# Kernel tuning notes

Hardware: AMD Instinct MI355X
Metric: run time of the kernel (lower is better)

## Reference

```python
import jax, jax.numpy as jnp
import numpy as np

B, L, HID, H, D = 16, 512, 768, 12, 64
NUM_STRUCT = 5


def setup_inputs() -> dict:
    key = jax.random.key(0)
    ks = jax.random.split(key, 8)
    hidden_states = jax.random.normal(ks[0], (B, L, HID), jnp.float32)
    attention_mask = jnp.zeros((B, 1, 1, L), jnp.float32)  # additive mask (0 = keep)
    structure_mask = (jax.random.uniform(ks[1], (NUM_STRUCT, B, 1, L, L)) < 0.15).astype(jnp.float32)
    s = 1.0 / np.sqrt(HID).astype(np.float32)
    Wq = jax.random.normal(ks[2], (HID, HID), jnp.float32) * s
    Wk = jax.random.normal(ks[3], (HID, HID), jnp.float32) * s
    Wv = jax.random.normal(ks[4], (HID, HID), jnp.float32) * s
    bq = jnp.zeros((HID,), jnp.float32)
    bk = jnp.zeros((HID,), jnp.float32)
    bv = jnp.zeros((HID,), jnp.float32)
    # xavier-uniform-ish scale for [D,D] biaffine mats
    xav = np.sqrt(6.0 / (D + D)).astype(np.float32)
    bili = jax.random.uniform(ks[5], (NUM_STRUCT, H, D, D), jnp.float32, -xav, xav)
    abs_bias = jnp.zeros((NUM_STRUCT, H), jnp.float32)
    return {"hidden_states": hidden_states, "attention_mask": attention_mask,
            "structure_mask": structure_mask, "Wq": Wq, "bq": bq, "Wk": Wk,
            "bk": bk, "Wv": Wv, "bv": bv, "bili": bili, "abs_bias": abs_bias}


def _heads(x, b, l):
    # [B,L,HID] -> [B,H,L,D]
    return x.reshape(b, l, H, D).transpose(0, 2, 1, 3)


def reference(hidden_states, attention_mask, structure_mask, Wq, bq, Wk, bk, Wv, bv, bili, abs_bias):
    b, l, _ = hidden_states.shape
    q = _heads(hidden_states @ Wq.T + bq, b, l)  # [B,H,L,D]
    k = _heads(hidden_states @ Wk.T + bk, b, l)
    v = _heads(hidden_states @ Wv.T + bv, b, l)

    scores = jnp.einsum('bhid,bhjd->bhij', q, k)  # [B,H,L,L]
    for i in range(NUM_STRUCT):
        bias = jnp.einsum('bhip,hpq,bhjq->bhij', q, bili[i], k)
        scores = scores + (bias + abs_bias[i][None, :, None, None]) * structure_mask[i]

    scores = scores / np.sqrt(D).astype(np.float32) + attention_mask
    probs = jax.nn.softmax(scores, axis=-1)
    ctx = jnp.einsum('bhij,bhjd->bhid', probs, v)  # [B,H,L,D]
    return ctx.transpose(0, 2, 1, 3).reshape(b, l, H * D)
```

## Files before the change

kernel.cpp:

```cpp
#include <hip/hip_runtime.h>
#include <hip/hip_bf16.h>

#define BATCH 16
#define SEQ   512
#define HID   768
#define NH    12
#define HD    64
#define NS    5

typedef __attribute__((ext_vector_type(8))) short short8;
typedef __attribute__((ext_vector_type(4))) float floatx4;

#define MFMA16(a, b, c) __builtin_amdgcn_mfma_f32_16x16x32_bf16((a), (b), (c), 0, 0, 0)

static __device__ __forceinline__ short f2bs(float f) {
    unsigned x = __builtin_bit_cast(unsigned, f);
    unsigned r = (x + 0x7fffu + ((x >> 16) & 1u)) >> 16;
    return (short)r;
}

__global__ void cvt_kernel(const float* __restrict__ src, short* __restrict__ dst, int n8) {
    int i = blockIdx.x * 256 + threadIdx.x;
    if (i >= n8) return;
    float4 a = ((const float4*)src)[2 * i];
    float4 b = ((const float4*)src)[2 * i + 1];
    short8 o;
    o[0] = f2bs(a.x); o[1] = f2bs(a.y); o[2] = f2bs(a.z); o[3] = f2bs(a.w);
    o[4] = f2bs(b.x); o[5] = f2bs(b.y); o[6] = f2bs(b.z); o[7] = f2bs(b.w);
    ((short8*)dst)[i] = o;
}

__global__ void bilit_kernel(const float* __restrict__ bili, short* __restrict__ bt) {
    int sh = blockIdx.x;
    const float* src = bili + (size_t)sh * 4096;
    short* dst = bt + (size_t)sh * 4096;
    for (int t = threadIdx.x; t < 4096; t += 256) {
        int p = t >> 6, qq = t & 63;
        dst[qq * 64 + p] = f2bs(src[p * 64 + qq]);
    }
}

__global__ void pack_mask_kernel(const float* __restrict__ smask, unsigned char* __restrict__ mp) {
    int idx = blockIdx.x * 256 + threadIdx.x;
    const size_t BLL = (size_t)BATCH * SEQ * SEQ;
    unsigned m = 0;
#pragma unroll
    for (int s = 0; s < NS; ++s)
        m |= (smask[(size_t)s * BLL + idx] != 0.f) ? (1u << s) : 0u;
    mp[idx] = (unsigned char)m;
}

__global__ __launch_bounds__(256) void proj_mfma(
    const short* __restrict__ xb, const short* __restrict__ Wb,
    const float* __restrict__ bq, const float* __restrict__ bk, const float* __restrict__ bv,
    short* __restrict__ qo, short* __restrict__ ko, short* __restrict__ vto)
{
    __shared__ short As[64 * 40];
    __shared__ short Bs[64 * 40];

    const int tid = threadIdx.x;
    const int m0 = blockIdx.x * 64;
    const int mh = blockIdx.y;
    const int mat = mh / NH, h = mh % NH;
    const short* Wm = Wb + (size_t)mat * HID * HID + (size_t)h * 64 * HID;
    const float* bias = (mat == 0) ? bq : (mat == 1) ? bk : bv;

    const int lane = tid & 63, w = tid >> 6;
    const int q4 = lane >> 4, c15 = lane & 15;
    const int srow = tid >> 2, skq = (tid & 3) * 8;

    floatx4 acc[4] = {{0.f,0.f,0.f,0.f},{0.f,0.f,0.f,0.f},{0.f,0.f,0.f,0.f},{0.f,0.f,0.f,0.f}};

    for (int k0 = 0; k0 < HID; k0 += 32) {
        *(short8*)&As[srow * 40 + skq] = *(const short8*)&xb[(size_t)(m0 + srow) * HID + k0 + skq];
        *(short8*)&Bs[srow * 40 + skq] = *(const short8*)&Wm[(size_t)srow * HID + k0 + skq];
        __syncthreads();
        short8 a = *(const short8*)&As[(w * 16 + c15) * 40 + q4 * 8];
#pragma unroll
        for (int c = 0; c < 4; ++c) {
            short8 bfr = *(const short8*)&Bs[(c * 16 + c15) * 40 + q4 * 8];
            acc[c] = MFMA16(a, bfr, acc[c]);
        }
        __syncthreads();
    }

    const int mg0 = m0 + w * 16 + q4 * 4;
    const int bb = mg0 >> 9, l0 = mg0 & 511;
#pragma unroll
    for (int c = 0; c < 4; ++c) {
        float bvv = bias[h * 64 + c * 16 + c15];
        if (mat < 2) {
            short* dst = (mat == 0) ? qo : ko;
#pragma unroll
            for (int r = 0; r < 4; ++r)
                dst[(((size_t)bb * NH + h) * SEQ + (l0 + r)) * HD + c * 16 + c15] = f2bs(acc[c][r] + bvv);
        } else {
            unsigned u0 = (unsigned short)f2bs(acc[c][0] + bvv) | ((unsigned)(unsigned short)f2bs(acc[c][1] + bvv) << 16);
            unsigned u1 = (unsigned short)f2bs(acc[c][2] + bvv) | ((unsigned)(unsigned short)f2bs(acc[c][3] + bvv) << 16);
            uint2 pk; pk.x = u0; pk.y = u1;
            *(uint2*)&vto[(((size_t)bb * NH + h) * HD + c * 16 + c15) * SEQ + l0] = pk;
        }
    }
}

__global__ __launch_bounds__(256, 3) void attn_mfma(
    const short* __restrict__ q, const short* __restrict__ k, const short* __restrict__ vt,
    const unsigned char* __restrict__ mp, const float* __restrict__ amask,
    const short* __restrict__ bilit, const float* __restrict__ abs_bias,
    float* __restrict__ out)
{
    __shared__ short Qs[64 * 72];
    __shared__ short Ks[64 * 72];
    __shared__ short Vs[64 * 72];
    __shared__ short Ps[64 * 72];

    const int it = blockIdx.x, h = blockIdx.y, b = blockIdx.z;
    const int i0 = it * 64;
    const int tid = threadIdx.x, lane = tid & 63, w = tid >> 6;
    const int q4 = lane >> 4, c15 = lane & 15;

    const size_t bh = (size_t)b * NH + h;
    const short* qg = q + bh * SEQ * HD;
    const short* kg = k + bh * SEQ * HD;
    const short* vg = vt + bh * HD * SEQ;

    for (int c = tid; c < 512; c += 256) {
        int r = c >> 3, o = (c & 7) * 8;
        *(short8*)&Qs[r * 72 + o] = *(const short8*)&qg[(size_t)(i0 + r) * HD + o];
    }
    float ab[NS];
#pragma unroll
    for (int s = 0; s < NS; ++s) ab[s] = abs_bias[s * NH + h];
    __syncthreads();

    short8 aQ0 = *(const short8*)&Qs[(w * 16 + c15) * 72 + q4 * 8];
    short8 aQ1 = *(const short8*)&Qs[(w * 16 + c15) * 72 + 32 + q4 * 8];

    short8 aP[NS][2];
    for (int s = 0; s < NS; ++s) {
        __syncthreads();
        const short* bt = bilit + ((size_t)s * NH + h) * 4096;
        for (int c = tid; c < 512; c += 256) {
            int r = c >> 3, o = (c & 7) * 8;
            *(short8*)&Ks[r * 72 + o] = *(const short8*)&bt[r * 64 + o];
        }
        __syncthreads();
#pragma unroll
        for (int ns = 0; ns < 4; ++ns) {
            short8 bf0 = *(const short8*)&Ks[(ns * 16 + c15) * 72 + q4 * 8];
            short8 bf1 = *(const short8*)&Ks[(ns * 16 + c15) * 72 + 32 + q4 * 8];
            floatx4 acc = {0.f, 0.f, 0.f, 0.f};
            acc = MFMA16(aQ0, bf0, acc);
            acc = MFMA16(aQ1, bf1, acc);
#pragma unroll
            for (int r = 0; r < 4; ++r)
                Ps[(w * 16 + q4 * 4 + r) * 72 + ns * 16 + c15] = f2bs(acc[r]);
        }
        aP[s][0] = *(const short8*)&Ps[(w * 16 + c15) * 72 + q4 * 8];
        aP[s][1] = *(const short8*)&Ps[(w * 16 + c15) * 72 + 32 + q4 * 8];
    }

    float m_r[4], l_r[4];
    floatx4 O[4];
#pragma unroll
    for (int r = 0; r < 4; ++r) { m_r[r] = -1e30f; l_r[r] = 0.f; }
#pragma unroll
    for (int d = 0; d < 4; ++d) O[d] = (floatx4){0.f, 0.f, 0.f, 0.f};

    const size_t mbase = (size_t)b * SEQ * SEQ;
    const int ibase = i0 + w * 16 + q4 * 4;

    for (int jt = 0; jt < 8; ++jt) {
        const int j0 = jt * 64;
        __syncthreads();
        for (int c = tid; c < 512; c += 256) {
            int r = c >> 3, o = (c & 7) * 8;
            *(short8*)&Ks[r * 72 + o] = *(const short8*)&kg[(size_t)(j0 + r) * HD + o];
            *(short8*)&Vs[r * 72 + o] = *(const short8*)&vg[(size_t)r * SEQ + j0 + o];
        }
        __syncthreads();

        float sv[4][4];
#pragma unroll
        for (int js = 0; js < 4; ++js) {
            const int jg = j0 + js * 16 + c15;
            unsigned mb[4];
#pragma unroll
            for (int r = 0; r < 4; ++r)
                mb[r] = mp[mbase + (size_t)(ibase + r) * SEQ + jg];
            float am = amask[b * SEQ + jg];

            short8 bf0 = *(const short8*)&Ks[(js * 16 + c15) * 72 + q4 * 8];
            short8 bf1 = *(const short8*)&Ks[(js * 16 + c15) * 72 + 32 + q4 * 8];
            floatx4 a0 = {0.f, 0.f, 0.f, 0.f};
            a0 = MFMA16(aQ0, bf0, a0);
            a0 = MFMA16(aQ1, bf1, a0);
            floatx4 as_[NS];
#pragma unroll
            for (int s = 0; s < NS; ++s) {
                floatx4 t = {0.f, 0.f, 0.f, 0.f};
                t = MFMA16(aP[s][0], bf0, t);
                t = MFMA16(aP[s][1], bf1, t);
                as_[s] = t;
            }
#pragma unroll
            for (int r = 0; r < 4; ++r) {
                float sc = a0[r];
#pragma unroll
                for (int s = 0; s < NS; ++s) {
                    float bit = (float)((mb[r] >> s) & 1u);
                    sc += bit * (as_[s][r] + ab[s]);
                }
                sv[js][r] = sc * 0.125f + am;
            }
        }

#pragma unroll
        for (int r = 0; r < 4; ++r) {
            float mx = fmaxf(fmaxf(sv[0][r], sv[1][r]), fmaxf(sv[2][r], sv[3][r]));
            mx = fmaxf(mx, __shfl_xor(mx, 1));
            mx = fmaxf(mx, __shfl_xor(mx, 2));
            mx = fmaxf(mx, __shfl_xor(mx, 4));
            mx = fmaxf(mx, __shfl_xor(mx, 8));
            float mn = fmaxf(m_r[r], mx);
            float alpha = __expf(m_r[r] - mn);
            m_r[r] = mn;
            float rs = 0.f;
#pragma unroll
            for (int js = 0; js < 4; ++js) {
                float p = __expf(sv[js][r] - mn);
                sv[js][r] = p;
                rs += p;
            }
            rs += __shfl_xor(rs, 1);
            rs += __shfl_xor(rs, 2);
            rs += __shfl_xor(rs, 4);
            rs += __shfl_xor(rs, 8);
            l_r[r] = l_r[r] * alpha + rs;
#pragma unroll
            for (int d = 0; d < 4; ++d) O[d][r] *= alpha;
        }

#pragma unroll
        for (int js = 0; js < 4; ++js)
#pragma unroll
            for (int r = 0; r < 4; ++r)
                Ps[(w * 16 + q4 * 4 + r) * 72 + js * 16 + c15] = f2bs(sv[js][r]);

        short8 pA0 = *(const short8*)&Ps[(w * 16 + c15) * 72 + q4 * 8];
        short8 pA1 = *(const short8*)&Ps[(w * 16 + c15) * 72 + 32 + q4 * 8];
#pragma unroll
        for (int d = 0; d < 4; ++d) {
            short8 vb0 = *(const short8*)&Vs[(d * 16 + c15) * 72 + q4 * 8];
            short8 vb1 = *(const short8*)&Vs[(d * 16 + c15) * 72 + 32 + q4 * 8];
            O[d] = MFMA16(pA0, vb0, O[d]);
            O[d] = MFMA16(pA1, vb1, O[d]);
        }
    }

#pragma unroll
    for (int r = 0; r < 4; ++r) {
        float inv = 1.f / l_r[r];
        int i = ibase + r;
        float* orow = out + ((size_t)b * SEQ + i) * HID + h * HD;
#pragma unroll
        for (int d = 0; d < 4; ++d)
            orow[d * 16 + c15] = O[d][r] * inv;
    }
}

extern "C" void kernel_launch(void* const* d_in, const int* in_sizes, int n_in,
                              void* d_out, int out_size, void* d_ws, size_t ws_size,
                              hipStream_t stream) {
    const float* hidden   = (const float*)d_in[0];
    const float* amask    = (const float*)d_in[1];
    const float* smask    = (const float*)d_in[2];
    const float* Wq       = (const float*)d_in[3];
    const float* bq       = (const float*)d_in[4];
    const float* Wk       = (const float*)d_in[5];
    const float* bk       = (const float*)d_in[6];
    const float* Wv       = (const float*)d_in[7];
    const float* bv       = (const float*)d_in[8];
    const float* bili     = (const float*)d_in[9];
    const float* abs_bias = (const float*)d_in[10];
    float* out = (float*)d_out;

    char* ws = (char*)d_ws;
    const size_t QKV = (size_t)BATCH * NH * SEQ * HD * 2;
    short* qb   = (short*)(ws);
    short* kb   = (short*)(ws + QKV);
    short* vtb  = (short*)(ws + 2 * QKV);
    short* xb   = (short*)(ws + 3 * QKV);
    short* Wb   = (short*)(ws + 4 * QKV);
    short* bltb = (short*)(ws + 4 * QKV + (size_t)3 * HID * HID * 2);
    unsigned char* mpk = (unsigned char*)(ws + 4 * QKV + (size_t)3 * HID * HID * 2
                                          + (size_t)NS * NH * HD * HD * 2);

    cvt_kernel<<<(BATCH * SEQ * HID / 8 + 255) / 256, 256, 0, stream>>>(hidden, xb, BATCH * SEQ * HID / 8);
    cvt_kernel<<<(HID * HID / 8 + 255) / 256, 256, 0, stream>>>(Wq, Wb, HID * HID / 8);
    cvt_kernel<<<(HID * HID / 8 + 255) / 256, 256, 0, stream>>>(Wk, Wb + (size_t)HID * HID, HID * HID / 8);
    cvt_kernel<<<(HID * HID / 8 + 255) / 256, 256, 0, stream>>>(Wv, Wb + (size_t)2 * HID * HID, HID * HID / 8);
    bilit_kernel<<<NS * NH, 256, 0, stream>>>(bili, bltb);
    pack_mask_kernel<<<BATCH * SEQ * SEQ / 256, 256, 0, stream>>>(smask, mpk);

    proj_mfma<<<dim3(BATCH * SEQ / 64, 3 * NH), 256, 0, stream>>>(xb, Wb, bq, bk, bv, qb, kb, vtb);

    attn_mfma<<<dim3(SEQ / 64, NH, BATCH), 256, 0, stream>>>(qb, kb, vtb, mpk, amask, bltb, abs_bias, out);
}
```

Baseline: 355.4 us.

## Retile projection GEMM, widen attention key tiles, vectorize mask packing, fold scales

The QKV projection moves from 64x64 tiles to 128x128 tiles per block, with a 4x4 MFMA grid per wave and direct global-to-LDS loads. The attention kernel now processes 128-key tiles, reuses one LDS buffer for Q, P and probabilities, and folds the 1/sqrt(D) scale into Q. The absolute biases are precomputed into a 32-entry lookup table indexed by the mask bits. Mask packing reads float4 and writes uchar4, and the three weight conversions are merged into one launch. Together these aim to cut global traffic, launch count and ALU work in the score loop, at the cost of more registers and LDS per block and possible occupancy loss.

```diff
diff --git a/kernel.cpp b/kernel.cpp
--- a/kernel.cpp
+++ b/kernel.cpp
@@ -13,10 +13,13 @@
 
 #define MFMA16(a, b, c) __builtin_amdgcn_mfma_f32_16x16x32_bf16((a), (b), (c), 0, 0, 0)
 
+#define GLOAD16(gp, lp) __builtin_amdgcn_global_load_lds( \
+    (const __attribute__((address_space(1))) unsigned*)(gp), \
+    (__attribute__((address_space(3))) unsigned*)(lp), 16, 0, 0)
+
 static __device__ __forceinline__ short f2bs(float f) {
     unsigned x = __builtin_bit_cast(unsigned, f);
-    unsigned r = (x + 0x7fffu + ((x >> 16) & 1u)) >> 16;
-    return (short)r;
+    return (short)((x + 0x7fffu + ((x >> 16) & 1u)) >> 16);
 }
 
 __global__ void cvt_kernel(const float* __restrict__ src, short* __restrict__ dst, int n8) {
@@ -30,6 +33,19 @@
     ((short8*)dst)[i] = o;
 }
 
+__global__ void cvtW_kernel(const float* __restrict__ wq, const float* __restrict__ wk,
+                            const float* __restrict__ wv, short* __restrict__ dst) {
+    const float* src = (blockIdx.y == 0) ? wq : (blockIdx.y == 1) ? wk : wv;
+    int i = blockIdx.x * 256 + threadIdx.x;
+    if (i >= HID * HID / 8) return;
+    float4 a = ((const float4*)src)[2 * i];
+    float4 b = ((const float4*)src)[2 * i + 1];
+    short8 o;
+    o[0] = f2bs(a.x); o[1] = f2bs(a.y); o[2] = f2bs(a.z); o[3] = f2bs(a.w);
+    o[4] = f2bs(b.x); o[5] = f2bs(b.y); o[6] = f2bs(b.z); o[7] = f2bs(b.w);
+    ((short8*)(dst + (size_t)blockIdx.y * HID * HID))[i] = o;
+}
+
 __global__ void bilit_kernel(const float* __restrict__ bili, short* __restrict__ bt) {
     int sh = blockIdx.x;
     const float* src = bili + (size_t)sh * 4096;
@@ -40,14 +56,20 @@
     }
 }
 
-__global__ void pack_mask_kernel(const float* __restrict__ smask, unsigned char* __restrict__ mp) {
-    int idx = blockIdx.x * 256 + threadIdx.x;
-    const size_t BLL = (size_t)BATCH * SEQ * SEQ;
-    unsigned m = 0;
-#pragma unroll
-    for (int s = 0; s < NS; ++s)
-        m |= (smask[(size_t)s * BLL + idx] != 0.f) ? (1u << s) : 0u;
-    mp[idx] = (unsigned char)m;
+__global__ void pack_mask_kernel(const float* __restrict__ smask, uchar4* __restrict__ mp) {
+    int i = blockIdx.x * 256 + threadIdx.x;
+    const size_t BLL4 = (size_t)BATCH * SEQ * SEQ / 4;
+    const float4* f = (const float4*)smask;
+    unsigned b0 = 0, b1 = 0, b2 = 0, b3 = 0;
+#pragma unroll
+    for (int s = 0; s < NS; ++s) {
+        float4 v = f[(size_t)s * BLL4 + i];
+        b0 |= (v.x != 0.f) ? (1u << s) : 0u;
+        b1 |= (v.y != 0.f) ? (1u << s) : 0u;
+        b2 |= (v.z != 0.f) ? (1u << s) : 0u;
+        b3 |= (v.w != 0.f) ? (1u << s) : 0u;
+    }
+    mp[i] = make_uchar4((unsigned char)b0, (unsigned char)b1, (unsigned char)b2, (unsigned char)b3);
 }
 
 __global__ __launch_bounds__(256) void proj_mfma(
@@ -55,64 +77,93 @@
     const float* __restrict__ bq, const float* __restrict__ bk, const float* __restrict__ bv,
     short* __restrict__ qo, short* __restrict__ ko, short* __restrict__ vto)
 {
-    __shared__ short As[64 * 40];
-    __shared__ short Bs[64 * 40];
-
-    const int tid = threadIdx.x;
-    const int m0 = blockIdx.x * 64;
-    const int mh = blockIdx.y;
-    const int mat = mh / NH, h = mh % NH;
-    const short* Wm = Wb + (size_t)mat * HID * HID + (size_t)h * 64 * HID;
-    const float* bias = (mat == 0) ? bq : (mat == 1) ? bk : bv;
-
-    const int lane = tid & 63, w = tid >> 6;
+    __shared__ short As[128 * 32];
+    __shared__ short Bs[128 * 32];
+
+    const int tid = threadIdx.x, lane = tid & 63, w = tid >> 6;
     const int q4 = lane >> 4, c15 = lane & 15;
-    const int srow = tid >> 2, skq = (tid & 3) * 8;
-
-    floatx4 acc[4] = {{0.f,0.f,0.f,0.f},{0.f,0.f,0.f,0.f},{0.f,0.f,0.f,0.f},{0.f,0.f,0.f,0.f}};
+    const int m0 = blockIdx.x * 128, n0 = blockIdx.y * 128;
+    const int wrow = (w & 1) * 64, wcol = (w >> 1) * 64;
+
+    const int srow = lane >> 2;
+    const int scol = (lane & 3) * 8;
+    const short* gA = xb + (size_t)(m0 + w * 32 + srow) * HID + scol;
+    const short* gB = Wb + (size_t)(n0 + w * 32 + srow) * HID + scol;
+    short* lA = As + w * 1024;
+    short* lB = Bs + w * 1024;
+
+    floatx4 acc[4][4];
+#pragma unroll
+    for (int i = 0; i < 4; ++i)
+#pragma unroll
+        for (int j = 0; j < 4; ++j) acc[i][j] = (floatx4){0.f, 0.f, 0.f, 0.f};
 
     for (int k0 = 0; k0 < HID; k0 += 32) {
-        *(short8*)&As[srow * 40 + skq] = *(const short8*)&xb[(size_t)(m0 + srow) * HID + k0 + skq];
-        *(short8*)&Bs[srow * 40 + skq] = *(const short8*)&Wm[(size_t)srow * HID + k0 + skq];
-        __syncthreads();
-        short8 a = *(const short8*)&As[(w * 16 + c15) * 40 + q4 * 8];
-#pragma unroll
-        for (int c = 0; c < 4; ++c) {
-            short8 bfr = *(const short8*)&Bs[(c * 16 + c15) * 40 + q4 * 8];
-            acc[c] = MFMA16(a, bfr, acc[c]);
-        }
-        __syncthreads();
-    }
-
-    const int mg0 = m0 + w * 16 + q4 * 4;
-    const int bb = mg0 >> 9, l0 = mg0 & 511;
-#pragma unroll
-    for (int c = 0; c < 4; ++c) {
-        float bvv = bias[h * 64 + c * 16 + c15];
-        if (mat < 2) {
-            short* dst = (mat == 0) ? qo : ko;
-#pragma unroll
-            for (int r = 0; r < 4; ++r)
-                dst[(((size_t)bb * NH + h) * SEQ + (l0 + r)) * HD + c * 16 + c15] = f2bs(acc[c][r] + bvv);
-        } else {
-            unsigned u0 = (unsigned short)f2bs(acc[c][0] + bvv) | ((unsigned)(unsigned short)f2bs(acc[c][1] + bvv) << 16);
-            unsigned u1 = (unsigned short)f2bs(acc[c][2] + bvv) | ((unsigned)(unsigned short)f2bs(acc[c][3] + bvv) << 16);
-            uint2 pk; pk.x = u0; pk.y = u1;
-            *(uint2*)&vto[(((size_t)bb * NH + h) * HD + c * 16 + c15) * SEQ + l0] = pk;
-        }
-    }
-}
-
-__global__ __launch_bounds__(256, 3) void attn_mfma(
+        __syncthreads();
+        GLOAD16(gA + k0,             lA);
+        GLOAD16(gA + k0 + 16 * HID,  lA + 512);
+        GLOAD16(gB + k0,             lB);
+        GLOAD16(gB + k0 + 16 * HID,  lB + 512);
+        __syncthreads();
+
+        short8 af[4], bf[4];
+#pragma unroll
+        for (int ri = 0; ri < 4; ++ri)
+            af[ri] = *(const short8*)&As[(wrow + ri * 16 + c15) * 32 + q4 * 8];
+#pragma unroll
+        for (int ci = 0; ci < 4; ++ci)
+            bf[ci] = *(const short8*)&Bs[(wcol + ci * 16 + c15) * 32 + q4 * 8];
+#pragma unroll
+        for (int ri = 0; ri < 4; ++ri)
+#pragma unroll
+            for (int ci = 0; ci < 4; ++ci)
+                acc[ri][ci] = MFMA16(af[ri], bf[ci], acc[ri][ci]);
+    }
+
+    const int matq = n0 / HID;
+    const float* bias = (matq == 0) ? bq : (matq == 1) ? bk : bv;
+
+#pragma unroll
+    for (int ci = 0; ci < 4; ++ci) {
+        const int nm = (n0 - matq * HID) + wcol + ci * 16 + c15;
+        const int h = nm >> 6, d = nm & 63;
+        const float bvv = bias[nm];
+#pragma unroll
+        for (int ri = 0; ri < 4; ++ri) {
+            const int mg0 = m0 + wrow + ri * 16 + q4 * 4;
+            const int bb = mg0 >> 9, l0 = mg0 & 511;
+            if (matq == 0) {
+#pragma unroll
+                for (int r = 0; r < 4; ++r)
+                    qo[(((size_t)bb * NH + h) * SEQ + (l0 + r)) * HD + d] =
+                        f2bs((acc[ri][ci][r] + bvv) * 0.125f);
+            } else if (matq == 1) {
+#pragma unroll
+                for (int r = 0; r < 4; ++r)
+                    ko[(((size_t)bb * NH + h) * SEQ + (l0 + r)) * HD + d] =
+                        f2bs(acc[ri][ci][r] + bvv);
+            } else {
+                unsigned u0 = (unsigned short)f2bs(acc[ri][ci][0] + bvv) |
+                              ((unsigned)(unsigned short)f2bs(acc[ri][ci][1] + bvv) << 16);
+                unsigned u1 = (unsigned short)f2bs(acc[ri][ci][2] + bvv) |
+                              ((unsigned)(unsigned short)f2bs(acc[ri][ci][3] + bvv) << 16);
+                uint2 pk; pk.x = u0; pk.y = u1;
+                *(uint2*)&vto[(((size_t)bb * NH + h) * HD + d) * SEQ + l0] = pk;
+            }
+        }
+    }
+}
+
+__global__ __launch_bounds__(256) void attn_mfma(
     const short* __restrict__ q, const short* __restrict__ k, const short* __restrict__ vt,
     const unsigned char* __restrict__ mp, const float* __restrict__ amask,
     const short* __restrict__ bilit, const float* __restrict__ abs_bias,
     float* __restrict__ out)
 {
-    __shared__ short Qs[64 * 72];
-    __shared__ short Ks[64 * 72];
-    __shared__ short Vs[64 * 72];
-    __shared__ short Ps[64 * 72];
+    __shared__ short U0[64 * 136];
+    __shared__ short Ks[128 * 72];
+    __shared__ short Vs[64 * 136];
+    __shared__ float abt[32];
 
     const int it = blockIdx.x, h = blockIdx.y, b = blockIdx.z;
     const int i0 = it * 64;
@@ -124,17 +175,21 @@
     const short* kg = k + bh * SEQ * HD;
     const short* vg = vt + bh * HD * SEQ;
 
+    if (tid < 32) {
+        float a = 0.f;
+#pragma unroll
+        for (int s = 0; s < NS; ++s)
+            if (tid & (1u << s)) a += abs_bias[s * NH + h];
+        abt[tid] = a * 0.125f;
+    }
+
     for (int c = tid; c < 512; c += 256) {
         int r = c >> 3, o = (c & 7) * 8;
-        *(short8*)&Qs[r * 72 + o] = *(const short8*)&qg[(size_t)(i0 + r) * HD + o];
-    }
-    float ab[NS];
-#pragma unroll
-    for (int s = 0; s < NS; ++s) ab[s] = abs_bias[s * NH + h];
+        *(short8*)&U0[r * 72 + o] = *(const short8*)&qg[(size_t)(i0 + r) * HD + o];
+    }
     __syncthreads();
-
-    short8 aQ0 = *(const short8*)&Qs[(w * 16 + c15) * 72 + q4 * 8];
-    short8 aQ1 = *(const short8*)&Qs[(w * 16 + c15) * 72 + 32 + q4 * 8];
+    short8 aQ0 = *(const short8*)&U0[(w * 16 + c15) * 72 + q4 * 8];
+    short8 aQ1 = *(const short8*)&U0[(w * 16 + c15) * 72 + 32 + q4 * 8];
 
     short8 aP[NS][2];
     for (int s = 0; s < NS; ++s) {
@@ -154,10 +209,10 @@
             acc = MFMA16(aQ1, bf1, acc);
 #pragma unroll
             for (int r = 0; r < 4; ++r)
-                Ps[(w * 16 + q4 * 4 + r) * 72 + ns * 16 + c15] = f2bs(acc[r]);
-        }
-        aP[s][0] = *(const short8*)&Ps[(w * 16 + c15) * 72 + q4 * 8];
-        aP[s][1] = *(const short8*)&Ps[(w * 16 + c15) * 72 + 32 + q4 * 8];
+                U0[(w * 16 + q4 * 4 + r) * 136 + ns * 16 + c15] = f2bs(acc[r]);
+        }
+        aP[s][0] = *(const short8*)&U0[(w * 16 + c15) * 136 + q4 * 8];
+        aP[s][1] = *(const short8*)&U0[(w * 16 + c15) * 136 + 32 + q4 * 8];
     }
 
     float m_r[4], l_r[4];
@@ -167,31 +222,31 @@
 #pragma unroll
     for (int d = 0; d < 4; ++d) O[d] = (floatx4){0.f, 0.f, 0.f, 0.f};
 
-    const size_t mbase = (size_t)b * SEQ * SEQ;
     const int ibase = i0 + w * 16 + q4 * 4;
-
-    for (int jt = 0; jt < 8; ++jt) {
-        const int j0 = jt * 64;
-        __syncthreads();
-        for (int c = tid; c < 512; c += 256) {
+    const unsigned char* rowp[4];
+#pragma unroll
+    for (int r = 0; r < 4; ++r)
+        rowp[r] = mp + (size_t)b * SEQ * SEQ + (size_t)(ibase + r) * SEQ + c15;
+    const float* amrow = amask + b * SEQ;
+
+    for (int jt = 0; jt < 4; ++jt) {
+        const int j0 = jt * 128;
+        __syncthreads();
+        for (int c = tid; c < 1024; c += 256) {
             int r = c >> 3, o = (c & 7) * 8;
             *(short8*)&Ks[r * 72 + o] = *(const short8*)&kg[(size_t)(j0 + r) * HD + o];
-            *(short8*)&Vs[r * 72 + o] = *(const short8*)&vg[(size_t)r * SEQ + j0 + o];
-        }
-        __syncthreads();
-
-        float sv[4][4];
-#pragma unroll
-        for (int js = 0; js < 4; ++js) {
-            const int jg = j0 + js * 16 + c15;
-            unsigned mb[4];
-#pragma unroll
-            for (int r = 0; r < 4; ++r)
-                mb[r] = mp[mbase + (size_t)(ibase + r) * SEQ + jg];
-            float am = amask[b * SEQ + jg];
-
-            short8 bf0 = *(const short8*)&Ks[(js * 16 + c15) * 72 + q4 * 8];
-            short8 bf1 = *(const short8*)&Ks[(js * 16 + c15) * 72 + 32 + q4 * 8];
+        }
+        for (int c = tid; c < 1024; c += 256) {
+            int d = c >> 4, o = (c & 15) * 8;
+            *(short8*)&Vs[d * 136 + o] = *(const short8*)&vg[(size_t)d * SEQ + j0 + o];
+        }
+        __syncthreads();
+
+        float sv[8][4];
+#pragma unroll
+        for (int js = 0; js < 8; ++js) {
+            const short8 bf0 = *(const short8*)&Ks[(js * 16 + c15) * 72 + q4 * 8];
+            const short8 bf1 = *(const short8*)&Ks[(js * 16 + c15) * 72 + 32 + q4 * 8];
             floatx4 a0 = {0.f, 0.f, 0.f, 0.f};
             a0 = MFMA16(aQ0, bf0, a0);
             a0 = MFMA16(aQ1, bf1, a0);
@@ -203,21 +258,23 @@
                 t = MFMA16(aP[s][1], bf1, t);
                 as_[s] = t;
             }
+            const float am = amrow[j0 + js * 16 + c15];
 #pragma unroll
             for (int r = 0; r < 4; ++r) {
-                float sc = a0[r];
-#pragma unroll
-                for (int s = 0; s < NS; ++s) {
-                    float bit = (float)((mb[r] >> s) & 1u);
-                    sc += bit * (as_[s][r] + ab[s]);
-                }
-                sv[js][r] = sc * 0.125f + am;
+                unsigned mb = rowp[r][j0 + js * 16];
+                float sc = a0[r] + am + abt[mb & 31];
+#pragma unroll
+                for (int s = 0; s < NS; ++s)
+                    sc = fmaf((float)((mb >> s) & 1u), as_[s][r], sc);
+                sv[js][r] = sc;
             }
         }
 
 #pragma unroll
         for (int r = 0; r < 4; ++r) {
-            float mx = fmaxf(fmaxf(sv[0][r], sv[1][r]), fmaxf(sv[2][r], sv[3][r]));
+            float mx = sv[0][r];
+#pragma unroll
+            for (int js = 1; js < 8; ++js) mx = fmaxf(mx, sv[js][r]);
             mx = fmaxf(mx, __shfl_xor(mx, 1));
             mx = fmaxf(mx, __shfl_xor(mx, 2));
             mx = fmaxf(mx, __shfl_xor(mx, 4));
@@ -227,7 +284,7 @@
             m_r[r] = mn;
             float rs = 0.f;
 #pragma unroll
-            for (int js = 0; js < 4; ++js) {
+            for (int js = 0; js < 8; ++js) {
                 float p = __expf(sv[js][r] - mn);
                 sv[js][r] = p;
                 rs += p;
@@ -242,27 +299,26 @@
         }
 
 #pragma unroll
-        for (int js = 0; js < 4; ++js)
+        for (int js = 0; js < 8; ++js)
 #pragma unroll
             for (int r = 0; r < 4; ++r)
-                Ps[(w * 16 + q4 * 4 + r) * 72 + js * 16 + c15] = f2bs(sv[js][r]);
-
-        short8 pA0 = *(const short8*)&Ps[(w * 16 + c15) * 72 + q4 * 8];
-        short8 pA1 = *(const short8*)&Ps[(w * 16 + c15) * 72 + 32 + q4 * 8];
-#pragma unroll
-        for (int d = 0; d < 4; ++d) {
-            short8 vb0 = *(const short8*)&Vs[(d * 16 + c15) * 72 + q4 * 8];
-            short8 vb1 = *(const short8*)&Vs[(d * 16 + c15) * 72 + 32 + q4 * 8];
-            O[d] = MFMA16(pA0, vb0, O[d]);
-            O[d] = MFMA16(pA1, vb1, O[d]);
+                U0[(w * 16 + q4 * 4 + r) * 136 + js * 16 + c15] = f2bs(sv[js][r]);
+
+#pragma unroll
+        for (int kk = 0; kk < 4; ++kk) {
+            short8 pA = *(const short8*)&U0[(w * 16 + c15) * 136 + kk * 32 + q4 * 8];
+#pragma unroll
+            for (int d = 0; d < 4; ++d) {
+                short8 vb = *(const short8*)&Vs[(d * 16 + c15) * 136 + kk * 32 + q4 * 8];
+                O[d] = MFMA16(pA, vb, O[d]);
+            }
         }
     }
 
 #pragma unroll
     for (int r = 0; r < 4; ++r) {
         float inv = 1.f / l_r[r];
-        int i = ibase + r;
-        float* orow = out + ((size_t)b * SEQ + i) * HID + h * HD;
+        float* orow = out + ((size_t)b * SEQ + ibase + r) * HID + h * HD;
 #pragma unroll
         for (int d = 0; d < 4; ++d)
             orow[d * 16 + c15] = O[d][r] * inv;
@@ -297,13 +353,13 @@
                                           + (size_t)NS * NH * HD * HD * 2);
 
     cvt_kernel<<<(BATCH * SEQ * HID / 8 + 255) / 256, 256, 0, stream>>>(hidden, xb, BATCH * SEQ * HID / 8);
-    cvt_kernel<<<(HID * HID / 8 + 255) / 256, 256, 0, stream>>>(Wq, Wb, HID * HID / 8);
-    cvt_kernel<<<(HID * HID / 8 + 255) / 256, 256, 0, stream>>>(Wk, Wb + (size_t)HID * HID, HID * HID / 8);
-    cvt_kernel<<<(HID * HID / 8 + 255) / 256, 256, 0, stream>>>(Wv, Wb + (size_t)2 * HID * HID, HID * HID / 8);
+    cvtW_kernel<<<dim3((HID * HID / 8 + 255) / 256, 3), 256, 0, stream>>>(Wq, Wk, Wv, Wb);
     bilit_kernel<<<NS * NH, 256, 0, stream>>>(bili, bltb);
-    pack_mask_kernel<<<BATCH * SEQ * SEQ / 256, 256, 0, stream>>>(smask, mpk);
-
-    proj_mfma<<<dim3(BATCH * SEQ / 64, 3 * NH), 256, 0, stream>>>(xb, Wb, bq, bk, bv, qb, kb, vtb);
-
-    attn_mfma<<<dim3(SEQ / 64, NH, BATCH), 256, 0, stream>>>(qb, kb, vtb, mpk, amask, bltb, abs_bias, out);
-}
+    pack_mask_kernel<<<BATCH * SEQ * SEQ / 4 / 256, 256, 0, stream>>>(smask, (uchar4*)mpk);
+
+    proj_mfma<<<dim3(BATCH * SEQ / 128, 3 * HID / 128), 256, 0, stream>>>(
+        xb, Wb, bq, bk, bv, qb, kb, vtb);
+
+    attn_mfma<<<dim3(SEQ / 64, NH, BATCH), 256, 0, stream>>>(
+        qb, kb, vtb, mpk, amask, bltb, abs_bias, out);
+}
```

New measurement: 353.7 us. Within noise of the previous version (-0.5%).
